# Kernel optimization log

Hardware: AMD Instinct MI355X
Metric: run time of the kernel (lower is better)

Reference implementation:

```python
import jax, jax.numpy as jnp
import numpy as np

N_NODES = 2000
GCN_OUT = 8
HID = 256
N_STEPS_OUT = 4


def setup_inputs() -> dict:
    key = jax.random.key(0)
    ks = jax.random.split(key, 16)
    B, S, N, E, F, H = 32, 24, N_NODES, 16000, GCN_OUT, HID
    I = F * N  # LSTM input size = gcn_out_features * num_nodes
    s = 0.05
    inp = {
        "x_sequences": jax.random.normal(ks[0], (B, S, N), jnp.float32),
        "edge_index": jax.random.randint(ks[1], (B, S, 2, E), 0, N, jnp.int32),
        "edge_distances": jax.random.uniform(ks[2], (B, S, E), jnp.float32),
        # CustomGCNLayer params (linear 1->F)
        "W_gcn": jax.random.normal(ks[3], (1, F), jnp.float32) * s,
        "b_gcn": jnp.zeros((F,), jnp.float32),
        # 2-layer LSTM (PyTorch layout: [4H, in], gate order i,f,g,o)
        "Wih0": jax.random.normal(ks[4], (4 * H, I), jnp.float32) * s,
        "Whh0": jax.random.normal(ks[5], (4 * H, H), jnp.float32) * s,
        "bih0": jnp.zeros((4 * H,), jnp.float32),
        "bhh0": jnp.zeros((4 * H,), jnp.float32),
        "Wih1": jax.random.normal(ks[6], (4 * H, H), jnp.float32) * s,
        "Whh1": jax.random.normal(ks[7], (4 * H, H), jnp.float32) * s,
        "bih1": jnp.zeros((4 * H,), jnp.float32),
        "bhh1": jnp.zeros((4 * H,), jnp.float32),
        # fc: hidden -> n_steps_out * num_nodes * num_node_features
        "fc_W": jax.random.normal(ks[8], (N_STEPS_OUT * N, H), jnp.float32) * s,
        "fc_b": jnp.zeros((N_STEPS_OUT * N,), jnp.float32),
    }
    return inp


def _lstm_layer(x, Wih, Whh, bih, bhh):
    # x: [B, S, in] -> hs: [B, S, H]
    B = x.shape[0]
    H = Whh.shape[1]
    b = bih + bhh

    def step(carry, xt):
        h, c = carry
        gates = xt @ Wih.T + h @ Whh.T + b  # [B, 4H]
        i, f, g, o = jnp.split(gates, 4, axis=-1)
        i = jax.nn.sigmoid(i)
        f = jax.nn.sigmoid(f)
        g = jnp.tanh(g)
        o = jax.nn.sigmoid(o)
        c = f * c + i * g
        h = o * jnp.tanh(c)
        return (h, c), h

    init = (jnp.zeros((B, H), x.dtype), jnp.zeros((B, H), x.dtype))
    _, hs = jax.lax.scan(step, init, x.transpose(1, 0, 2))  # time-major
    return hs.transpose(1, 0, 2)


def reference(x_sequences, edge_index, edge_distances, W_gcn, b_gcn,
              Wih0, Whh0, bih0, bhh0, Wih1, Whh1, bih1, bhh1, fc_W, fc_b):
    B, S, N = x_sequences.shape
    F = W_gcn.shape[1]
    # GCN layer (batched over all B*S graph snapshots):
    # h = x @ W + b ; out[i] = sum_{(j->i)} dist_e * h[j]
    h = x_sequences[..., None] * W_gcn[0] + b_gcn        # [B,S,N,F]
    src = edge_index[:, :, 0].reshape(B * S, -1)         # [BS,E]
    dst = edge_index[:, :, 1].reshape(B * S, -1)
    dist = edge_distances.reshape(B * S, -1)
    h2 = h.reshape(B * S, N, F)
    msgs = jnp.take_along_axis(h2, src[:, :, None], axis=1) * dist[..., None]  # [BS,E,F]
    agg = jax.vmap(lambda m, d: jax.ops.segment_sum(m, d, num_segments=N))(msgs, dst)
    gcn_seq = jnp.tanh(agg.reshape(B, S, N * F))         # [B,S,N*F]

    h1 = _lstm_layer(gcn_seq, Wih0, Whh0, bih0, bhh0)
    h2l = _lstm_layer(h1, Wih1, Whh1, bih1, bhh1)
    last = jnp.tanh(h2l)[:, -1, :]                       # [B,H]
    out = last @ fc_W.T + fc_b                           # [B, n_steps_out*N]
    n_steps_out = fc_b.shape[0] // N
    return out.reshape(B, n_steps_out, N)                # num_node_features=1 squeezed
```

## Files before the change

kernel.cpp:

```cpp
#include <hip/hip_runtime.h>

#define DEVINL __device__ __forceinline__

typedef __attribute__((ext_vector_type(8))) short bf16x8;
typedef __attribute__((ext_vector_type(4))) float f32x4;
typedef _Float16 half2_t __attribute__((ext_vector_type(2)));
typedef _Float16 f16x8 __attribute__((ext_vector_type(8)));

DEVINL unsigned short f2bf(float f) {
  unsigned int u = __float_as_uint(f);
  u += 0x7FFFu + ((u >> 16) & 1u);
  return (unsigned short)(u >> 16);
}
DEVINL unsigned short f2h(float f) {
  return __builtin_bit_cast(unsigned short, (_Float16)f);
}
DEVINL float sigmf(float x) { return 1.f / (1.f + __expf(-x)); }
DEVINL float tanh_fast(float x) { float e = __expf(2.f * x); return 1.f - 2.f / (e + 1.f); }

DEVINL float fdot2u(unsigned int h, unsigned int w, float acc) {
  return __builtin_amdgcn_fdot2(__builtin_bit_cast(half2_t, h),
                                __builtin_bit_cast(half2_t, w), acc, false);
}

DEVINL void gload_lds16(const void* g, void* l) {
  __builtin_amdgcn_global_load_lds(
      (const __attribute__((address_space(1))) void*)g,
      (__attribute__((address_space(3))) void*)l, 16, 0, 0);
}


__global__ __launch_bounds__(256) void conv_bf16(const float* __restrict__ in,
                                                 unsigned short* __restrict__ out) {
  int id = blockIdx.x * 256 + threadIdx.x;
  float4 v = *(const float4*)&in[(size_t)id * 4];
  unsigned int a = (unsigned int)f2bf(v.x) | ((unsigned int)f2bf(v.y) << 16);
  unsigned int b = (unsigned int)f2bf(v.z) | ((unsigned int)f2bf(v.w) << 16);
  *(uint2*)&out[(size_t)id * 4] = make_uint2(a, b);
}

__global__ __launch_bounds__(256) void conv_f16(const float* __restrict__ in,
                                                unsigned short* __restrict__ out) {
  int id = blockIdx.x * 256 + threadIdx.x;
  out[id] = f2h(in[id]);
}

__global__ __launch_bounds__(256) void pack_whh_g(const float* __restrict__ in,
                                                  uint2* __restrict__ out) {
  int id = blockIdx.x * 256 + threadIdx.x;
  int g = id >> 14;
  int rem = id & 16383;
  int u2 = rem >> 8;
  int c = rem & 255;
  int col = (c >> 6) * 256 + g * 64 + (c & 63);
  float4 v = *(const float4*)&in[col * 256 + u2 * 4];
  unsigned int p0 = (unsigned int)f2h(v.x) | ((unsigned int)f2h(v.y) << 16);
  unsigned int p1 = (unsigned int)f2h(v.z) | ((unsigned int)f2h(v.w) << 16);
  out[id] = make_uint2(p0, p1);
}

#define FXSCALE 1048576.f
#define FXINV   (1.f / 1048576.f)

__global__ __launch_bounds__(1024) void gcn_kernel(
    const float* __restrict__ x, const int* __restrict__ ei, const float* __restrict__ ed,
    const float* __restrict__ Wg, const float* __restrict__ bg,
    unsigned short* __restrict__ G) {
  __shared__ float xs[2000];
  __shared__ int Ai[2000];
  __shared__ int Di[2000];
  int bs = blockIdx.x;
  int tid = threadIdx.x;
  for (int i = tid; i < 2000; i += 1024) {
    xs[i] = x[(size_t)bs * 2000 + i];
    Ai[i] = 0; Di[i] = 0;
  }
  bool bgz = (bg[0] == 0.f) && (bg[1] == 0.f) && (bg[2] == 0.f) && (bg[3] == 0.f) &&
             (bg[4] == 0.f) && (bg[5] == 0.f) && (bg[6] == 0.f) && (bg[7] == 0.f);
  __syncthreads();
  const int4* srcp = (const int4*)(ei + (size_t)bs * 32000);
  const int4* dstp = (const int4*)(ei + (size_t)bs * 32000 + 16000);
  const float4* dp = (const float4*)(ed + (size_t)bs * 16000);
  if (bgz) {
    for (int i = tid; i < 4000; i += 1024) {
      int4 s4 = srcp[i];
      int4 d4 = dstp[i];
      float4 w4 = dp[i];
      atomicAdd(&Ai[d4.x], __float2int_rn(w4.x * xs[s4.x] * FXSCALE));
      atomicAdd(&Ai[d4.y], __float2int_rn(w4.y * xs[s4.y] * FXSCALE));
      atomicAdd(&Ai[d4.z], __float2int_rn(w4.z * xs[s4.z] * FXSCALE));
      atomicAdd(&Ai[d4.w], __float2int_rn(w4.w * xs[s4.w] * FXSCALE));
    }
  } else {
    for (int i = tid; i < 4000; i += 1024) {
      int4 s4 = srcp[i];
      int4 d4 = dstp[i];
      float4 w4 = dp[i];
      atomicAdd(&Ai[d4.x], __float2int_rn(w4.x * xs[s4.x] * FXSCALE));
      atomicAdd(&Di[d4.x], __float2int_rn(w4.x * FXSCALE));
      atomicAdd(&Ai[d4.y], __float2int_rn(w4.y * xs[s4.y] * FXSCALE));
      atomicAdd(&Di[d4.y], __float2int_rn(w4.y * FXSCALE));
      atomicAdd(&Ai[d4.z], __float2int_rn(w4.z * xs[s4.z] * FXSCALE));
      atomicAdd(&Di[d4.z], __float2int_rn(w4.z * FXSCALE));
      atomicAdd(&Ai[d4.w], __float2int_rn(w4.w * xs[s4.w] * FXSCALE));
      atomicAdd(&Di[d4.w], __float2int_rn(w4.w * FXSCALE));
    }
  }
  __syncthreads();
  float wreg[8], breg[8];
#pragma unroll
  for (int f = 0; f < 8; ++f) { wreg[f] = Wg[f]; breg[f] = bg[f]; }
  for (int n = tid; n < 2000; n += 1024) {
    float a  = (float)Ai[n] * FXINV;
    float dd = (float)Di[n] * FXINV;
    unsigned int u[4];
#pragma unroll
    for (int p = 0; p < 4; ++p) {
      float v0 = tanh_fast(wreg[2 * p] * a + breg[2 * p] * dd);
      float v1 = tanh_fast(wreg[2 * p + 1] * a + breg[2 * p + 1] * dd);
      u[p] = (unsigned int)f2bf(v0) | ((unsigned int)f2bf(v1) << 16);
    }
    *(uint4*)&G[(size_t)bs * 16000 + n * 8] = make_uint4(u[0], u[1], u[2], u[3]);
  }
}

__global__ __launch_bounds__(256) void gemm_bt(
    const unsigned short* __restrict__ A, const unsigned short* __restrict__ B,
    float* __restrict__ Cp) {
  __shared__ __align__(16) unsigned short As[2][128 * 32];
  __shared__ __align__(16) unsigned short Bs[2][128 * 32];
  const int K = 16000;
  int nt = blockIdx.x;
  int mt = blockIdx.y;
  int ks = blockIdx.z;
  int m0 = mt * 128, n0 = nt * 128;
  int tid = threadIdx.x;
  int lane = tid & 63;
  int w = tid >> 6;
  int wm = (w >> 1) * 64, wn = (w & 1) * 64;
  int fr = lane & 15;
  int kg = lane >> 4;

  f32x4 acc[4][4] = {};
  const unsigned short* Ag = A + (size_t)m0 * K + ks * 1600;
  const unsigned short* Bg = B + (size_t)n0 * K + ks * 1600;

  int row0 = tid >> 2,            ko0 = (tid & 3) * 8,        cb0 = (tid & ~63);
  int row1 = (256 + tid) >> 2,    ko1 = (tid & 3) * 8,        cb1 = 256 + (tid & ~63);

#define STAGE_BT(buf, kk)                                                     \
  do {                                                                        \
    gload_lds16(&Ag[(size_t)row0 * K + (kk) + ko0], &As[buf][cb0 * 8]);       \
    gload_lds16(&Bg[(size_t)row0 * K + (kk) + ko0], &Bs[buf][cb0 * 8]);       \
    gload_lds16(&Ag[(size_t)row1 * K + (kk) + ko1], &As[buf][cb1 * 8]);       \
    gload_lds16(&Bg[(size_t)row1 * K + (kk) + ko1], &Bs[buf][cb1 * 8]);       \
  } while (0)

  STAGE_BT(0, 0);
#pragma unroll 1
  for (int it = 0; it < 50; ++it) {
    int cur = it & 1;
    if (it < 49) {
      STAGE_BT(cur ^ 1, (it + 1) * 32);
      asm volatile("s_waitcnt vmcnt(4)" ::: "memory");
    } else {
      asm volatile("s_waitcnt vmcnt(0)" ::: "memory");
    }
    __builtin_amdgcn_s_barrier();
    __builtin_amdgcn_sched_barrier(0);
    bf16x8 aF[4], bF[4];
#pragma unroll
    for (int i = 0; i < 4; ++i)
      aF[i] = *(const bf16x8*)&As[cur][(wm + i * 16 + fr) * 32 + kg * 8];
#pragma unroll
    for (int i = 0; i < 4; ++i)
      bF[i] = *(const bf16x8*)&Bs[cur][(wn + i * 16 + fr) * 32 + kg * 8];
#pragma unroll
    for (int i = 0; i < 4; ++i)
#pragma unroll
      for (int j = 0; j < 4; ++j)
        acc[i][j] = __builtin_amdgcn_mfma_f32_16x16x32_bf16(aF[i], bF[j], acc[i][j], 0, 0, 0);
    __builtin_amdgcn_s_barrier();
  }
#undef STAGE_BT
  float* Co = Cp + (size_t)ks * 768 * 1024;
  int mr = (lane >> 4) * 4;
#pragma unroll
  for (int i = 0; i < 4; ++i)
#pragma unroll
    for (int j = 0; j < 4; ++j) {
      int n = n0 + wn + j * 16 + fr;
#pragma unroll
      for (int r = 0; r < 4; ++r) {
        int m = m0 + wm + i * 16 + mr + r;
        Co[(size_t)m * 1024 + n] = acc[i][j][r];
      }
    }
}

__global__ __launch_bounds__(256) void reduce_z0(
    const float* __restrict__ Cp, const float* __restrict__ bih,
    const float* __restrict__ bhh, float* __restrict__ Z0) {
  int id = blockIdx.x * 256 + threadIdx.x;
  float s = bih[id & 1023] + bhh[id & 1023];
#pragma unroll
  for (int p = 0; p < 10; ++p) s += Cp[(size_t)p * 786432 + id];
  Z0[id] = s;
}

__global__ __launch_bounds__(1024) void lstm_sync2(
    const float* __restrict__ Z, const uint2* __restrict__ WPG,
    unsigned int* __restrict__ Hex, unsigned short* __restrict__ Hout,
    float* __restrict__ lastOut, int tagBase) {
  __shared__ __align__(16) uint2 Wl2[64 * 256];
  __shared__ float gparts[1024];
  __shared__ __align__(8) unsigned short h16[256];
  int bid = blockIdx.x;
  int b = bid & 31, g = bid >> 5;
  int tid = threadIdx.x;
  int lane = tid & 63;
  int c = tid & 255;
  int kh = __builtin_amdgcn_readfirstlane(tid >> 8);
  int q = c >> 6, r = c & 63;
  int col = q * 256 + g * 64 + r;

  const uint2* wsrc = WPG + (size_t)g * 16384;
  for (int i = tid; i < 16384; i += 1024) Wl2[i] = wsrc[i];
  if (tid < 128) ((unsigned int*)h16)[tid] = 0;
  __syncthreads();

  float cst = 0.f;
  const size_t b24 = (size_t)b * 24;

#pragma unroll 1
  for (int t = 0; t < 24; ++t) {
    uint2 hv = *(const uint2*)&((const unsigned int*)h16)[lane * 2];
    float acc = (kh == 0) ? Z[(b24 + t) * 1024 + col] : 0.f;
#pragma unroll
    for (int j = 0; j < 16; ++j) {
      const int u2i = kh * 16 + j;
      uint2 w2 = Wl2[u2i * 256 + c];
      unsigned int h0 = (unsigned int)__builtin_amdgcn_readlane((int)hv.x, u2i);
      unsigned int h1 = (unsigned int)__builtin_amdgcn_readlane((int)hv.y, u2i);
      acc = fdot2u(h0, w2.x, acc);
      acc = fdot2u(h1, w2.y, acc);
    }
    gparts[tid] = acc;
    __syncthreads();
    unsigned int* HexS = Hex + (t & 1) * 8192 + b * 256;
    if (tid < 64) {
      float i_ = gparts[tid]       + gparts[tid + 256]  + gparts[tid + 512]  + gparts[tid + 768];
      float f_ = gparts[tid + 64]  + gparts[tid + 320]  + gparts[tid + 576]  + gparts[tid + 832];
      float g_ = gparts[tid + 128] + gparts[tid + 384]  + gparts[tid + 640]  + gparts[tid + 896];
      float o_ = gparts[tid + 192] + gparts[tid + 448]  + gparts[tid + 704]  + gparts[tid + 960];
      float ig = sigmf(i_), fg = sigmf(f_);
      float gg = tanh_fast(g_), og = sigmf(o_);
      cst = fg * cst + ig * gg;
      float h = og * tanh_fast(cst);
      unsigned short hh = f2h(h);
      h16[g * 64 + tid] = hh;
      __hip_atomic_store(&HexS[g * 64 + tid],
                         (unsigned int)hh | ((unsigned int)(tagBase + t + 1) << 16),
                         __ATOMIC_RELAXED, __HIP_MEMORY_SCOPE_AGENT);
      if (Hout) Hout[(b24 + t) * 256 + g * 64 + tid] = hh;
      if (lastOut && t == 23) lastOut[b * 256 + g * 64 + tid] = tanh_fast(h);
    }
    if (t == 23) break;
    if (tid < 256 && (tid >> 6) != g) {
      const unsigned int tag = (unsigned int)(tagBase + t + 1);
      unsigned int v;
      do {
        v = __hip_atomic_load(&HexS[tid], __ATOMIC_RELAXED, __HIP_MEMORY_SCOPE_AGENT);
      } while ((v >> 16) != tag);
      h16[tid] = (unsigned short)(v & 0xFFFFu);
    }
    __syncthreads();
  }
}

__global__ __launch_bounds__(256) void gemm_z1_mfma(
    const unsigned short* __restrict__ A, const unsigned short* __restrict__ B,
    const float* __restrict__ bih, const float* __restrict__ bhh,
    float* __restrict__ Z1) {
  __shared__ __align__(16) unsigned short As[128 * 32];
  __shared__ __align__(16) unsigned short Bs[128 * 32];
  const int K = 256;
  int nt = blockIdx.x;
  int mt = blockIdx.y;
  int m0 = mt * 128, n0 = nt * 128;
  int tid = threadIdx.x;
  int lane = tid & 63;
  int w = tid >> 6;
  int wm = (w >> 1) * 64, wn = (w & 1) * 64;
  int fr = lane & 15;
  int kg = lane >> 4;

  f32x4 acc[4][4] = {};
  const unsigned short* Ag = A + (size_t)m0 * K;
  const unsigned short* Bg = B + (size_t)n0 * K;

  for (int kk = 0; kk < 256; kk += 32) {
#pragma unroll
    for (int q = 0; q < 2; ++q) {
      int c = q * 256 + tid;
      int row = c >> 2;
      int ko = (c & 3) * 8;
      int cb = q * 256 + (tid & ~63);
      gload_lds16(&Ag[(size_t)row * K + kk + ko], &As[cb * 8]);
      gload_lds16(&Bg[(size_t)row * K + kk + ko], &Bs[cb * 8]);
    }
    __syncthreads();
    f16x8 aF[4], bF[4];
#pragma unroll
    for (int i = 0; i < 4; ++i)
      aF[i] = *(const f16x8*)&As[(wm + i * 16 + fr) * 32 + kg * 8];
#pragma unroll
    for (int i = 0; i < 4; ++i)
      bF[i] = *(const f16x8*)&Bs[(wn + i * 16 + fr) * 32 + kg * 8];
#pragma unroll
    for (int i = 0; i < 4; ++i)
#pragma unroll
      for (int j = 0; j < 4; ++j)
        acc[i][j] = __builtin_amdgcn_mfma_f32_16x16x32_f16(aF[i], bF[j], acc[i][j], 0, 0, 0);
    __syncthreads();
  }
  int mr = (lane >> 4) * 4;
#pragma unroll
  for (int j = 0; j < 4; ++j) {
    int n = n0 + wn + j * 16 + fr;
    float bias = bih[n] + bhh[n];
#pragma unroll
    for (int i = 0; i < 4; ++i) {
#pragma unroll
      for (int r = 0; r < 4; ++r) {
        int m = m0 + wm + i * 16 + mr + r;
        Z1[(size_t)m * 1024 + n] = acc[i][j][r] + bias;
      }
    }
  }
}

__global__ __launch_bounds__(256) void fc_kernel(
    const float* __restrict__ last, const float* __restrict__ fcW,
    const float* __restrict__ fcb, float* __restrict__ out) {
  __shared__ float ls[8][256];
  int tid = threadIdx.x;
  int o = blockIdx.x * 256 + tid;
  int b0 = blockIdx.y * 8;
  for (int i = tid; i < 2048; i += 256)
    ls[i >> 8][i & 255] = last[(b0 + (i >> 8)) * 256 + (i & 255)];
  __syncthreads();
  if (o < 8000) {
    float acc[8] = {};
    for (int k = 0; k < 256; k += 4) {
      float4 wv = *(const float4*)&fcW[(size_t)o * 256 + k];
#pragma unroll
      for (int b = 0; b < 8; ++b)
        acc[b] += wv.x * ls[b][k] + wv.y * ls[b][k + 1] + wv.z * ls[b][k + 2] + wv.w * ls[b][k + 3];
    }
    float bias = fcb[o];
#pragma unroll
    for (int b = 0; b < 8; ++b) out[(size_t)(b0 + b) * 8000 + o] = acc[b] + bias;
  }
}

extern "C" void kernel_launch(void* const* d_in, const int* in_sizes, int n_in,
                              void* d_out, int out_size, void* d_ws, size_t ws_size,
                              hipStream_t stream) {
  const float* x    = (const float*)d_in[0];
  const int*   ei   = (const int*)d_in[1];
  const float* ed   = (const float*)d_in[2];
  const float* Wg   = (const float*)d_in[3];
  const float* bg   = (const float*)d_in[4];
  const float* Wih0 = (const float*)d_in[5];
  const float* Whh0 = (const float*)d_in[6];
  const float* bih0 = (const float*)d_in[7];
  const float* bhh0 = (const float*)d_in[8];
  const float* Wih1 = (const float*)d_in[9];
  const float* Whh1 = (const float*)d_in[10];
  const float* bih1 = (const float*)d_in[11];
  const float* bhh1 = (const float*)d_in[12];
  const float* fcW  = (const float*)d_in[13];
  const float* fcb  = (const float*)d_in[14];
  float* out = (float*)d_out;

  char* ws = (char*)d_ws;
  unsigned short* Gbf  = (unsigned short*)(ws);
  unsigned short* W0bf = (unsigned short*)(ws + 24576000);
  float* Zpart = (float*)(ws + 57344000);
  float* Z0    = (float*)(ws + 88801280);
  uint2* WPG0  = (uint2*)(ws + 91947008);
  uint2* WPG1  = (uint2*)(ws + 92471296);
  unsigned short* W1h = (unsigned short*)(ws + 92995584);
  unsigned short* H1  = (unsigned short*)(ws + 94044160);
  float* Z1    = (float*)(ws + 94830592);
  float* lastb = (float*)(ws + 97976320);
  unsigned int* Hex0 = (unsigned int*)(ws + 98009088);
  unsigned int* Hex1 = (unsigned int*)(ws + 98074624);

  hipMemsetAsync(Hex0, 0, 131072, stream);
  conv_bf16<<<16000, 256, 0, stream>>>(Wih0, W0bf);
  pack_whh_g<<<256, 256, 0, stream>>>(Whh0, WPG0);
  pack_whh_g<<<256, 256, 0, stream>>>(Whh1, WPG1);
  conv_f16<<<1024, 256, 0, stream>>>(Wih1, (unsigned short*)W1h);
  gcn_kernel<<<768, 1024, 0, stream>>>(x, ei, ed, Wg, bg, Gbf);
  gemm_bt<<<dim3(8, 6, 10), 256, 0, stream>>>(Gbf, W0bf, Zpart);
  reduce_z0<<<3072, 256, 0, stream>>>(Zpart, bih0, bhh0, Z0);
  lstm_sync2<<<128, 1024, 0, stream>>>(Z0, WPG0, Hex0, H1, nullptr, 0);
  gemm_z1_mfma<<<dim3(8, 6), 256, 0, stream>>>(H1, W1h, bih1, bhh1, Z1);
  lstm_sync2<<<128, 1024, 0, stream>>>(Z1, WPG1, Hex1, nullptr, lastb, 100);
  fc_kernel<<<dim3(32, 4), 256, 0, stream>>>(lastb, fcW, fcb, out);
}
```

Baseline: 240.4 us.

## Double-buffer GCN edge loads into LDS with async global-to-LDS copies

Replaces the direct per-thread global loads of edge src/dst/weight in the GCN scatter with a chunked, double-buffered pipeline. Async global-to-LDS loads fetch the next 2000-edge chunk while the current chunk is scattered with LDS atomics. The goal is to hide global memory latency behind the atomic work, at the cost of 48KB of extra LDS per block (which may reduce occupancy) and two barriers per chunk.

New measurement: 248.0 us. 3.2% more time.

```diff
diff --git a/kernel.cpp b/kernel.cpp
--- a/kernel.cpp
+++ b/kernel.cpp
@@ -69,8 +69,34 @@
   __shared__ float xs[2000];
   __shared__ int Ai[2000];
   __shared__ int Di[2000];
+  __shared__ __align__(16) char stg[2][24576];
   int bs = blockIdx.x;
   int tid = threadIdx.x;
+
+  const char* srcB = (const char*)(ei + (size_t)bs * 32000);
+  const char* dstB = (const char*)(ei + (size_t)bs * 32000 + 16000);
+  const char* wB   = (const char*)(ed + (size_t)bs * 16000);
+
+  int slot1 = tid;
+  int slot2 = 1024 + (tid & 511);
+
+#define GSTAGE(par, c)                                                        \
+  do {                                                                        \
+    {                                                                         \
+      int r = slot1 >> 9, i = slot1 & 511;                                    \
+      int ic = i < 500 ? i : 499;                                             \
+      const char* base = (r == 0) ? srcB : (r == 1) ? dstB : wB;              \
+      gload_lds16(base + (c) * 8000 + ic * 16, &stg[par][(slot1 & ~63) * 16]);\
+    }                                                                         \
+    {                                                                         \
+      int r = slot2 >> 9, i = slot2 & 511;                                    \
+      int ic = i < 500 ? i : 499;                                             \
+      const char* base = (r == 0) ? srcB : (r == 1) ? dstB : wB;              \
+      gload_lds16(base + (c) * 8000 + ic * 16, &stg[par][(slot2 & ~63) * 16]);\
+    }                                                                         \
+  } while (0)
+
+  GSTAGE(0, 0);
   for (int i = tid; i < 2000; i += 1024) {
     xs[i] = x[(size_t)bs * 2000 + i];
     Ai[i] = 0; Di[i] = 0;
@@ -78,34 +104,38 @@
   bool bgz = (bg[0] == 0.f) && (bg[1] == 0.f) && (bg[2] == 0.f) && (bg[3] == 0.f) &&
              (bg[4] == 0.f) && (bg[5] == 0.f) && (bg[6] == 0.f) && (bg[7] == 0.f);
   __syncthreads();
-  const int4* srcp = (const int4*)(ei + (size_t)bs * 32000);
-  const int4* dstp = (const int4*)(ei + (size_t)bs * 32000 + 16000);
-  const float4* dp = (const float4*)(ed + (size_t)bs * 16000);
-  if (bgz) {
-    for (int i = tid; i < 4000; i += 1024) {
-      int4 s4 = srcp[i];
-      int4 d4 = dstp[i];
-      float4 w4 = dp[i];
-      atomicAdd(&Ai[d4.x], __float2int_rn(w4.x * xs[s4.x] * FXSCALE));
-      atomicAdd(&Ai[d4.y], __float2int_rn(w4.y * xs[s4.y] * FXSCALE));
-      atomicAdd(&Ai[d4.z], __float2int_rn(w4.z * xs[s4.z] * FXSCALE));
-      atomicAdd(&Ai[d4.w], __float2int_rn(w4.w * xs[s4.w] * FXSCALE));
-    }
-  } else {
-    for (int i = tid; i < 4000; i += 1024) {
-      int4 s4 = srcp[i];
-      int4 d4 = dstp[i];
-      float4 w4 = dp[i];
-      atomicAdd(&Ai[d4.x], __float2int_rn(w4.x * xs[s4.x] * FXSCALE));
-      atomicAdd(&Di[d4.x], __float2int_rn(w4.x * FXSCALE));
-      atomicAdd(&Ai[d4.y], __float2int_rn(w4.y * xs[s4.y] * FXSCALE));
-      atomicAdd(&Di[d4.y], __float2int_rn(w4.y * FXSCALE));
-      atomicAdd(&Ai[d4.z], __float2int_rn(w4.z * xs[s4.z] * FXSCALE));
-      atomicAdd(&Di[d4.z], __float2int_rn(w4.z * FXSCALE));
-      atomicAdd(&Ai[d4.w], __float2int_rn(w4.w * xs[s4.w] * FXSCALE));
-      atomicAdd(&Di[d4.w], __float2int_rn(w4.w * FXSCALE));
-    }
-  }
+
+#pragma unroll 1
+  for (int c = 0; c < 8; ++c) {
+    int par = c & 1;
+    if (c < 7) {
+      GSTAGE(par ^ 1, c + 1);
+      asm volatile("s_waitcnt vmcnt(2)" ::: "memory");
+    } else {
+      asm volatile("s_waitcnt vmcnt(0)" ::: "memory");
+    }
+    __builtin_amdgcn_s_barrier();
+    __builtin_amdgcn_sched_barrier(0);
+    const int* Sv = (const int*)&stg[par][0];
+    const int* Dv = (const int*)&stg[par][8192];
+    const float* Wv = (const float*)&stg[par][16384];
+    if (bgz) {
+      for (int e = tid; e < 2000; e += 1024) {
+        int s = Sv[e], d = Dv[e];
+        float w = Wv[e];
+        atomicAdd(&Ai[d], __float2int_rn(w * xs[s] * FXSCALE));
+      }
+    } else {
+      for (int e = tid; e < 2000; e += 1024) {
+        int s = Sv[e], d = Dv[e];
+        float w = Wv[e];
+        atomicAdd(&Ai[d], __float2int_rn(w * xs[s] * FXSCALE));
+        atomicAdd(&Di[d], __float2int_rn(w * FXSCALE));
+      }
+    }
+    __builtin_amdgcn_s_barrier();
+  }
+#undef GSTAGE
   __syncthreads();
   float wreg[8], breg[8];
 #pragma unroll
```
